# Kernel optimization log

Measured on AMD Instinct MI355X. Metric: run time of the kernel, lower is better.

## Reference

```python
import jax, jax.numpy as jnp
import numpy as np

H, DH = 6, 64
D = H * DH
SQRT_DH = np.float32(np.sqrt(DH))


def _pool_norm(tok, ids):
    # masked mean pooling over tokens, then L2 normalize (Encoder.mean_pooling + normalize)
    mask = (ids > 0).astype(tok.dtype)[:, :, None]
    s = jnp.sum(tok * mask, axis=1) / jnp.clip(jnp.sum(mask, axis=1), 1e-9, None)
    return s / jnp.clip(jnp.linalg.norm(s, axis=1, keepdims=True), 1e-12, None)


def setup_inputs() -> dict:
    key = jax.random.key(0)
    ks = jax.random.split(key, 16)
    N_MSG, N_CON, L, E = 10000, 20000, 16, 128000
    s = 0.05
    eye = jnp.eye(DH, dtype=jnp.float32)
    inp = {}
    inp['tok_msg'] = jax.random.normal(ks[0], (N_MSG, L, D), jnp.float32)
    inp['tok_con'] = jax.random.normal(ks[1], (N_CON, L, D), jnp.float32)
    inp['ids_msg'] = jax.random.randint(ks[2], (N_MSG, L), 0, 100)
    inp['ids_con'] = jax.random.randint(ks[3], (N_CON, L), 0, 100)
    inp['src_cm'] = jax.random.randint(ks[4], (E,), 0, N_CON)
    inp['dst_cm'] = jax.random.randint(ks[5], (E,), 0, N_MSG)
    inp['src_mc'] = jax.random.randint(ks[6], (E,), 0, N_MSG)
    inp['dst_mc'] = jax.random.randint(ks[7], (E,), 0, N_CON)
    inp['lin_W'] = jax.random.normal(ks[8], (2, D, D), jnp.float32) * s
    inp['lin_b'] = jnp.zeros((2, D), jnp.float32)
    inp['kW'] = jax.random.normal(ks[9], (2, 2, D, D), jnp.float32) * s
    inp['kb'] = jnp.zeros((2, 2, D), jnp.float32)
    inp['qW'] = jax.random.normal(ks[10], (2, 2, D, D), jnp.float32) * s
    inp['qb'] = jnp.zeros((2, 2, D), jnp.float32)
    inp['vW'] = jax.random.normal(ks[11], (2, 2, D, D), jnp.float32) * s
    inp['vb'] = jnp.zeros((2, 2, D), jnp.float32)
    inp['aW'] = jax.random.normal(ks[12], (2, 2, D, D), jnp.float32) * s
    inp['ab'] = jnp.zeros((2, 2, D), jnp.float32)
    inp['a_rel'] = jax.random.normal(ks[13], (2, 2, H, DH, DH), jnp.float32) * s + eye
    inp['m_rel'] = jax.random.normal(ks[14], (2, 2, H, DH, DH), jnp.float32) * s + eye
    inp['p_rel'] = jnp.ones((2, 2, H), jnp.float32)
    inp['skip'] = jnp.ones((2, 2), jnp.float32)
    return inp


def _hgt_layer(xs, edges, kW, kb, qW, qb, vW, vb, aW, ab, a_rel, m_rel, p_rel, skip):
    # xs = [x_message, x_concept]; edges = ((src, dst) per edge type)
    k = [(xs[t] @ kW[t] + kb[t]).reshape(-1, H, DH) for t in (0, 1)]
    q = [(xs[t] @ qW[t] + qb[t]).reshape(-1, H, DH) for t in (0, 1)]
    v = [(xs[t] @ vW[t] + vb[t]).reshape(-1, H, DH) for t in (0, 1)]
    edge_meta = ((1, 0), (0, 1))  # edge type e -> (src_type, dst_type)
    agg = [None, None]
    for e, (s, d) in enumerate(edge_meta):
        si, di = edges[e]
        Nd = xs[d].shape[0]
        # relation-specific key/message transforms, per head: [E, H, DH]
        ke = jnp.einsum('ehd,hdf->ehf', k[s][si], a_rel[e])
        score = jnp.einsum('ehf,ehf->eh', q[d][di], ke) * p_rel[e] / SQRT_DH
        # softmax over incoming edges per destination node
        m = jax.ops.segment_max(score, di, num_segments=Nd)
        ex = jnp.exp(score - m[di])
        den = jax.ops.segment_sum(ex, di, num_segments=Nd)
        alpha = ex / den[di]
        msg = jnp.einsum('ehd,hdf->ehf', v[s][si], m_rel[e]) * alpha[:, :, None]
        agg[d] = jax.ops.segment_sum(msg, di, num_segments=Nd).reshape(Nd, D)
    out = []
    for t in (0, 1):
        o = jax.nn.gelu(agg[t], approximate=False) @ aW[t] + ab[t]
        a = jax.nn.sigmoid(skip[t])
        out.append(a * o + (1.0 - a) * xs[t])
    return out


def reference(tok_msg, tok_con, ids_msg, ids_con, src_cm, dst_cm, src_mc, dst_mc,
              lin_W, lin_b, kW, kb, qW, qb, vW, vb, aW, ab, a_rel, m_rel, p_rel, skip):
    x0 = jax.nn.relu(_pool_norm(tok_msg, ids_msg) @ lin_W[0] + lin_b[0])
    x1 = jax.nn.relu(_pool_norm(tok_con, ids_con) @ lin_W[1] + lin_b[1])
    edges = ((src_cm, dst_cm), (src_mc, dst_mc))
    xs = [x0, x1]
    for l in range(2):  # num_layers = 2 (hard-coded in MedicalEncoder)
        xs = _hgt_layer(xs, edges, kW[l], kb[l], qW[l], qb[l], vW[l], vb[l],
                        aW[l], ab[l], a_rel[l], m_rel[l], p_rel[l], skip[l])
    return xs[0]  # x_dict['message']
```

## Files before the change

### kernel.cpp

```cpp
#include <hip/hip_runtime.h>
#include <math.h>

#define H 6
#define DH 64
#define D 384
#define L 16
#define WSZ ((size_t)(D) * (D))
#define RSZ ((size_t)(H) * (DH) * (DH))

typedef __attribute__((ext_vector_type(8))) short short8;
typedef __attribute__((ext_vector_type(4))) float f32x4;
typedef unsigned int uint_;

__device__ __forceinline__ float bf2f(unsigned short u) {
  union { unsigned int i; float f; } x; x.i = ((unsigned int)u) << 16; return x.f;
}
__device__ __forceinline__ unsigned short f2bf(float f) {
  unsigned int x = __float_as_uint(f);
  x = x + 0x7fffu + ((x >> 16) & 1u);
  return (unsigned short)(x >> 16);
}
__device__ __forceinline__ float blo(unsigned int u) { return __uint_as_float(u << 16); }
__device__ __forceinline__ float bhi(unsigned int u) { return __uint_as_float(u & 0xffff0000u); }
__device__ __forceinline__ float geluf(float x) {
  return 0.5f * x * (1.0f + erff(x * 0.70710678118654752f));
}

__global__ void zero_int_kernel(int* p, long n) {
  long i = (long)blockIdx.x * blockDim.x + threadIdx.x;
  long stride = (long)gridDim.x * blockDim.x;
  for (; i < n; i += stride) p[i] = 0;
}

__global__ __launch_bounds__(512) void poolprep_kernel(
    const float* __restrict__ tokM, const int* __restrict__ idsM,
    unsigned short* __restrict__ outM, int NM,
    const float* __restrict__ tokC, const int* __restrict__ idsC,
    unsigned short* __restrict__ outC, int NPOOL,
    const int* __restrict__ dc0, const int* __restrict__ dc1,
    int* __restrict__ deg0, int* __restrict__ deg1, int E, int CH,
    const float* __restrict__ lin_W, const float* __restrict__ kW,
    const float* __restrict__ qW, const float* __restrict__ vW,
    const float* __restrict__ aW, const float* __restrict__ a_rel,
    const float* __restrict__ m_rel, const float* __restrict__ p_rel,
    const float* __restrict__ kb, const float* __restrict__ qb,
    const float* __restrict__ vb,
    unsigned short* __restrict__ wbuf, float* __restrict__ bbuf) {
  __shared__ __align__(16) char smem[16768];
  int t = threadIdx.x;
  if ((int)blockIdx.x < NPOOL) {
    {
      int e = blockIdx.x * CH + t;
      if (t < CH && e < 2 * E) {
        if (e < E) atomicAdd(&deg0[dc0[e]], 1);
        else atomicAdd(&deg1[dc1[e - E]], 1);
      }
    }
    float4 (*part)[96] = (float4(*)[96])smem;
    float* wpart = (float*)(smem + 6144);
    int n = blockIdx.x;
    const float* tok; const int* ids; unsigned short* out;
    if (n < NM) { tok = tokM; ids = idsM; out = outM; }
    else { n -= NM; tok = tokC; ids = idsC; out = outC; }
    int rg = t / 96, c4 = t % 96;
    const float4* tp = (const float4*)(tok + (size_t)n * L * D);
    const int* ip = ids + (size_t)n * L;
    int cnt = 0;
#pragma unroll
    for (int l = 0; l < L; ++l) cnt += (ip[l] > 0);
    float4 s = {0.f, 0.f, 0.f, 0.f};
    if (t < 384) {
#pragma unroll
      for (int li = 0; li < 4; ++li) {
        int l = rg + li * 4;
        if (ip[l] > 0) {
          float4 v = tp[l * 96 + c4];
          s.x += v.x; s.y += v.y; s.z += v.z; s.w += v.w;
        }
      }
      part[rg][c4] = s;
    }
    __syncthreads();
    float4 m4 = {0.f, 0.f, 0.f, 0.f};
    float dot = 0.f;
    float inv_cnt = 1.0f / fmaxf((float)cnt, 1e-9f);
    if (t < 96) {
      float4 a = part[0][t], b = part[1][t], c = part[2][t], d2 = part[3][t];
      m4.x = (a.x + b.x + c.x + d2.x) * inv_cnt;
      m4.y = (a.y + b.y + c.y + d2.y) * inv_cnt;
      m4.z = (a.z + b.z + c.z + d2.z) * inv_cnt;
      m4.w = (a.w + b.w + c.w + d2.w) * inv_cnt;
      dot = m4.x * m4.x + m4.y * m4.y + m4.z * m4.z + m4.w * m4.w;
    }
#pragma unroll
    for (int o = 32; o; o >>= 1) dot += __shfl_down(dot, o);
    if ((t & 63) == 0) wpart[t >> 6] = dot;
    __syncthreads();
    float tot = 0.f;
#pragma unroll
    for (int i = 0; i < 8; ++i) tot += wpart[i];
    float inv = 1.0f / fmaxf(sqrtf(tot), 1e-12f);
    if (t < 96) {
      uint2 o;
      o.x = (uint_)f2bf(m4.x * inv) | ((uint_)f2bf(m4.y * inv) << 16);
      o.y = (uint_)f2bf(m4.z * inv) | ((uint_)f2bf(m4.w * inv) << 16);
      ((uint2*)(out + (size_t)n * D))[t] = o;
    }
    return;
  }
  int q = blockIdx.x - NPOOL;
  if (q >= 14 * 144) {
    int i = (q - 14 * 144) * 512 + t;
    if (i >= 3456) return;
    int gemm, col;
    if (i < 1152) { gemm = 0; col = i; }
    else if (i < 2304) { gemm = 1; col = i - 1152; }
    else if (i < 2688) { gemm = 2; col = i - 2304; }
    else { gemm = 3; col = i - 2688; }
    int sec = col / D, j = col % D, h = j >> 6, rr = j & 63;
    float out = 0.f;
    if (gemm == 0) {
      if (sec == 0) out = kb[j];
      else if (sec == 1) {
        const float* R = a_rel + (size_t)h * 4096 + (size_t)rr * 64;
        float s = 0.f; for (int f = 0; f < 64; ++f) s += qb[h * 64 + f] * R[f];
        out = s * p_rel[h] * 0.125f;
      } else {
        const float* Mm = m_rel + RSZ + (size_t)h * 4096;
        float s = 0.f; for (int d = 0; d < 64; ++d) s += vb[h * 64 + d] * Mm[d * 64 + rr]; out = s;
      }
    } else if (gemm == 1) {
      if (sec == 0) out = kb[D + j];
      else if (sec == 1) {
        const float* R = a_rel + RSZ + (size_t)h * 4096 + (size_t)rr * 64;
        float s = 0.f; for (int f = 0; f < 64; ++f) s += qb[D + h * 64 + f] * R[f];
        out = s * p_rel[H + h] * 0.125f;
      } else {
        const float* Mm = m_rel + (size_t)h * 4096;
        float s = 0.f; for (int d = 0; d < 64; ++d) s += vb[D + h * 64 + d] * Mm[d * 64 + rr]; out = s;
      }
    } else if (gemm == 2) {
      const float* R = a_rel + 2 * RSZ + (size_t)h * 4096 + (size_t)rr * 64;
      float s = 0.f; for (int f = 0; f < 64; ++f) s += qb[2 * D + h * 64 + f] * R[f];
      out = s * p_rel[2 * H + h] * 0.125f;
    } else {
      if (sec == 0) out = kb[3 * D + j];
      else {
        const float* Mm = m_rel + 2 * RSZ + (size_t)h * 4096;
        float s = 0.f; for (int d = 0; d < 64; ++d) s += vb[3 * D + h * 64 + d] * Mm[d * 64 + rr]; out = s;
      }
    }
    bbuf[i] = out;
    return;
  }
  int z = q / 144;
  int r = q % 144;
  int px = r % 12, py = r / 12;
  int tx = t & 31, ty16 = t >> 5;
  const float* src; const float* rel = nullptr; const float* prl = nullptr; int type = 0;
  switch (z) {
    case 0: src = lin_W; break;
    case 1: src = lin_W + WSZ; break;
    case 2: src = kW; break;
    case 3: type = 1; src = qW; rel = a_rel; prl = p_rel; break;
    case 4: type = 2; src = vW; rel = m_rel + RSZ; break;
    case 5: src = kW + WSZ; break;
    case 6: type = 1; src = qW + WSZ; rel = a_rel + RSZ; prl = p_rel + H; break;
    case 7: type = 2; src = vW + WSZ; rel = m_rel; break;
    case 8: type = 1; src = qW + 2 * WSZ; rel = a_rel + 2 * RSZ; prl = p_rel + 2 * H; break;
    case 9: src = kW + 3 * WSZ; break;
    case 10: type = 2; src = vW + 3 * WSZ; rel = m_rel + 2 * RSZ; break;
    case 11: src = aW; break;
    case 12: src = aW + WSZ; break;
    default: src = aW + 2 * WSZ; break;
  }
  unsigned short* dst = wbuf + (size_t)z * WSZ;
  int bx = px * 32;
  int by = py * 32;
  if (type == 0) {
    float (*tile)[33] = (float(*)[33])smem;
#pragma unroll
    for (int s = 0; s < 2; ++s) {
      int r2 = ty16 + s * 16;
      tile[r2][tx] = src[(size_t)(bx + r2) * D + by + tx];
    }
    __syncthreads();
#pragma unroll
    for (int s = 0; s < 2; ++s) {
      int ny = ty16 + s * 16;
      dst[(size_t)(by + ny) * D + bx + tx] = f2bf(tile[tx][ny]);
    }
  } else if (type == 1) {
    float (*Wt_)[65] = (float(*)[65])smem;
    float (*Rt)[65] = (float(*)[65])(smem + 8320);
    int h = by >> 6, d0 = by & 63;
    float sc = prl[h] * 0.125f;
#pragma unroll
    for (int i = 0; i < 4; ++i) {
      int idx = t + i * 512;
      int wr = idx >> 6, wc = idx & 63;
      Wt_[wr][wc] = src[(size_t)(bx + wr) * D + h * 64 + wc];
      Rt[wr][wc] = rel[(size_t)h * 4096 + (size_t)(d0 + wr) * 64 + wc];
    }
    __syncthreads();
#pragma unroll
    for (int s = 0; s < 2; ++s) {
      int ny = ty16 + s * 16;
      float acc = 0.f;
#pragma unroll 16
      for (int f = 0; f < 64; ++f) acc += Wt_[tx][f] * Rt[ny][f];
      dst[(size_t)(by + ny) * D + bx + tx] = f2bf(acc * sc);
    }
  } else {
    float (*Wt2)[65] = (float(*)[65])smem;
    float (*Mt)[33] = (float(*)[33])(smem + 8320);
    int h = by >> 6, f0 = by & 63;
#pragma unroll
    for (int i = 0; i < 4; ++i) {
      int idx = t + i * 512;
      int wr = idx >> 6, wc = idx & 63;
      Wt2[wr][wc] = src[(size_t)(bx + wr) * D + h * 64 + wc];
      int dr = idx >> 5, fc = idx & 31;
      Mt[dr][fc] = rel[(size_t)h * 4096 + (size_t)dr * 64 + f0 + fc];
    }
    __syncthreads();
#pragma unroll
    for (int s = 0; s < 2; ++s) {
      int ny = ty16 + s * 16;
      float acc = 0.f;
#pragma unroll 16
      for (int d = 0; d < 64; ++d) acc += Wt2[tx][d] * Mt[d][ny];
      dst[(size_t)(by + ny) * D + bx + tx] = f2bf(acc);
    }
  }
}

__global__ void scan2_kernel(const int* __restrict__ deg0, int* __restrict__ off0, int N0,
                             const int* __restrict__ deg1, int* __restrict__ off1, int N1) {
  const int* deg = blockIdx.x ? deg1 : deg0;
  int* off = blockIdx.x ? off1 : off0;
  int N = blockIdx.x ? N1 : N0;
  __shared__ int wsum[16];
  __shared__ int carrySh;
  int tid = threadIdx.x;
  int lane = tid & 63, wid = tid >> 6;
  if (tid == 0) carrySh = 0;
  __syncthreads();
  for (int base = 0; base < N; base += 1024) {
    int i = base + tid;
    int v = (i < N) ? deg[i] : 0;
    int s = v;
#pragma unroll
    for (int o = 1; o < 64; o <<= 1) {
      int t2 = __shfl_up(s, o);
      if (lane >= o) s += t2;
    }
    if (lane == 63) wsum[wid] = s;
    __syncthreads();
    int wpre = 0;
    for (int j = 0; j < wid; ++j) wpre += wsum[j];
    int c = carrySh;
    if (i < N) off[i] = c + wpre + s - v;
    __syncthreads();
    if (tid == 1023) carrySh = c + wpre + s;
    __syncthreads();
  }
  if (tid == 0) off[N] = carrySh;
}

struct AttnP {
  const unsigned short* kb;
  const unsigned short* tqb;
  const unsigned short* vmb;
  const int* off;
  const int* elist;
  unsigned short* aggb;
  int N, sk, st, sv, nb;
};

__global__ void attn_kernel(AttnP a0, AttnP a1) {
  bool first = (int)blockIdx.x < a0.nb;
  AttnP a = first ? a0 : a1;
  int bx = first ? (int)blockIdx.x : (int)blockIdx.x - a0.nb;
  int node = bx * 4 + (threadIdx.x >> 6);
  int lane = threadIdx.x & 63;
  if (node >= a.N) return;
  int e0 = a.off[node], e1 = a.off[node + 1];
  const uint_* tq32 = (const uint_*)(a.tqb + (size_t)node * a.st);
  float tq0[3], tq1[3], m[3], den[3], ac0[3], ac1[3];
#pragma unroll
  for (int j = 0; j < 3; ++j) {
    uint_ u = tq32[lane + 64 * j];
    tq0[j] = blo(u); tq1[j] = bhi(u);
    m[j] = -1e30f; den[j] = 0.f; ac0[j] = 0.f; ac1[j] = 0.f;
  }
  int i = e0;
  for (; i + 2 <= e1; i += 2) {
    int s0 = a.elist[i], s1 = a.elist[i + 1];
    const uint_* k0 = (const uint_*)(a.kb + (size_t)s0 * a.sk);
    const uint_* k1 = (const uint_*)(a.kb + (size_t)s1 * a.sk);
    const uint_* v0 = (const uint_*)(a.vmb + (size_t)s0 * a.sv);
    const uint_* v1 = (const uint_*)(a.vmb + (size_t)s1 * a.sv);
    float pa[3], pb[3]; uint_ va[3], vb[3];
#pragma unroll
    for (int j = 0; j < 3; ++j) {
      uint_ ka = k0[lane + 64 * j], kbu = k1[lane + 64 * j];
      va[j] = v0[lane + 64 * j]; vb[j] = v1[lane + 64 * j];
      pa[j] = blo(ka) * tq0[j] + bhi(ka) * tq1[j];
      pb[j] = blo(kbu) * tq0[j] + bhi(kbu) * tq1[j];
    }
#pragma unroll
    for (int o = 1; o <= 16; o <<= 1)
#pragma unroll
      for (int j = 0; j < 3; ++j) {
        pa[j] += __shfl_xor(pa[j], o);
        pb[j] += __shfl_xor(pb[j], o);
      }
#pragma unroll
    for (int j = 0; j < 3; ++j) {
      float mn = fmaxf(m[j], fmaxf(pa[j], pb[j]));
      float r = __expf(m[j] - mn);
      float p0 = __expf(pa[j] - mn);
      float p1 = __expf(pb[j] - mn);
      den[j] = den[j] * r + p0 + p1;
      ac0[j] = ac0[j] * r + p0 * blo(va[j]) + p1 * blo(vb[j]);
      ac1[j] = ac1[j] * r + p0 * bhi(va[j]) + p1 * bhi(vb[j]);
      m[j] = mn;
    }
  }
  if (i < e1) {
    int s0 = a.elist[i];
    const uint_* k0 = (const uint_*)(a.kb + (size_t)s0 * a.sk);
    const uint_* v0 = (const uint_*)(a.vmb + (size_t)s0 * a.sv);
    float pa[3]; uint_ va[3];
#pragma unroll
    for (int j = 0; j < 3; ++j) {
      uint_ ka = k0[lane + 64 * j];
      va[j] = v0[lane + 64 * j];
      pa[j] = blo(ka) * tq0[j] + bhi(ka) * tq1[j];
    }
#pragma unroll
    for (int o = 1; o <= 16; o <<= 1)
#pragma unroll
      for (int j = 0; j < 3; ++j) pa[j] += __shfl_xor(pa[j], o);
#pragma unroll
    for (int j = 0; j < 3; ++j) {
      float mn = fmaxf(m[j], pa[j]);
      float r = __expf(m[j] - mn);
      float p0 = __expf(pa[j] - mn);
      den[j] = den[j] * r + p0;
      ac0[j] = ac0[j] * r + p0 * blo(va[j]);
      ac1[j] = ac1[j] * r + p0 * bhi(va[j]);
      m[j] = mn;
    }
  }
  uint_* op32 = (uint_*)(a.aggb + (size_t)node * D);
#pragma unroll
  for (int j = 0; j < 3; ++j) {
    float o0 = (e1 > e0) ? ac0[j] / den[j] : 0.f;
    float o1 = (e1 > e0) ? ac1[j] / den[j] : 0.f;
    op32[lane + 64 * j] = (uint_)f2bf(geluf(o0)) | ((uint_)f2bf(geluf(o1)) << 16);
  }
}

struct GemmP {
  const unsigned short* A;
  const unsigned short* Wt;
  const float* bias;
  float* Cf;
  unsigned short* Cb;
  const unsigned short* xold;
  const float* skipPtr;
  int M, N, cpitch, relu;
};
struct ScatP {
  const int *d0, *s0, *off0;
  int *cur0, *el0;
  const int *d1, *s1, *off1;
  int *cur1, *el1;
  int E;
};

__global__ __launch_bounds__(256) void gemm_bf16(GemmP q0, GemmP q1, ScatP sc) {
  if (blockIdx.z == 2) {
    int nb = gridDim.x * gridDim.y;
    int flat = blockIdx.y * gridDim.x + blockIdx.x;
    for (int e = flat * 256 + threadIdx.x; e < 2 * sc.E; e += nb * 256) {
      if (e < sc.E) {
        int d = sc.d0[e];
        sc.el0[sc.off0[d] + atomicAdd(&sc.cur0[d], 1)] = sc.s0[e];
      } else {
        int ee = e - sc.E;
        int d = sc.d1[ee];
        sc.el1[sc.off1[d] + atomicAdd(&sc.cur1[d], 1)] = sc.s1[ee];
      }
    }
    return;
  }
  GemmP p = blockIdx.z ? q1 : q0;
  const int bm = blockIdx.x * 128, bn = blockIdx.y * 128;
  if (bm >= p.M || bn >= p.N) return;
  __shared__ __align__(16) unsigned short As[2][128 * 64];
  __shared__ __align__(16) unsigned short Bs[2][128 * 64];
  const int tid = threadIdx.x;
  const int w = tid >> 6, lane = tid & 63;

  auto stage = [&](int t, int buf) {
#pragma unroll
    for (int i = 0; i < 4; ++i) {
      int cid = (w * 4 + i) * 64 + lane;
      int row = cid >> 3;
      int cg = (cid & 7) ^ (row & 7);
      int grow = bm + row;
      if (grow >= p.M) grow = p.M - 1;
      const unsigned short* gp = p.A + (size_t)grow * D + t * 64 + cg * 8;
      __builtin_amdgcn_global_load_lds((const __attribute__((address_space(1))) void*)gp,
                                       (__attribute__((address_space(3))) void*)&As[buf][(w * 4 + i) * 512],
                                       16, 0, 0);
    }
#pragma unroll
    for (int i = 0; i < 4; ++i) {
      int cid = (w * 4 + i) * 64 + lane;
      int row = cid >> 3;
      int cg = (cid & 7) ^ (row & 7);
      const unsigned short* gp = p.Wt + (size_t)(bn + row) * D + t * 64 + cg * 8;
      __builtin_amdgcn_global_load_lds((const __attribute__((address_space(1))) void*)gp,
                                       (__attribute__((address_space(3))) void*)&Bs[buf][(w * 4 + i) * 512],
                                       16, 0, 0);
    }
  };

  stage(0, 0);
  __syncthreads();

  const int wr = w >> 1, wc = w & 1;
  const int la = lane & 15, hi = lane >> 4;
  f32x4 acc[4][4] = {};

  for (int t = 0; t < 6; ++t) {
    if (t < 5) stage(t + 1, (t + 1) & 1);
    const unsigned short* Ab = As[t & 1];
    const unsigned short* Bb = Bs[t & 1];
#pragma unroll
    for (int ks = 0; ks < 2; ++ks) {
      int c = ks * 4 + hi;
      short8 af[4], bfr[4];
#pragma unroll
      for (int mi = 0; mi < 4; ++mi) {
        int row = wr * 64 + mi * 16 + la;
        af[mi] = *(const short8*)&Ab[row * 64 + ((c ^ (row & 7)) * 8)];
      }
#pragma unroll
      for (int n = 0; n < 4; ++n) {
        int col = wc * 64 + n * 16 + la;
        bfr[n] = *(const short8*)&Bb[col * 64 + ((c ^ (col & 7)) * 8)];
      }
#pragma unroll
      for (int mi = 0; mi < 4; ++mi)
#pragma unroll
        for (int n = 0; n < 4; ++n)
          acc[mi][n] = __builtin_amdgcn_mfma_f32_16x16x32_bf16(af[mi], bfr[n], acc[mi][n], 0, 0, 0);
    }
    __syncthreads();
  }

  float sa = 0.f;
  if (p.xold) sa = 1.0f / (1.0f + __expf(-*p.skipPtr));
#pragma unroll
  for (int mi = 0; mi < 4; ++mi) {
#pragma unroll
    for (int n = 0; n < 4; ++n) {
#pragma unroll
      for (int r = 0; r < 4; ++r) {
        int row = bm + wr * 64 + mi * 16 + hi * 4 + r;
        int col = bn + wc * 64 + n * 16 + la;
        if (row >= p.M) continue;
        float v = acc[mi][n][r] + p.bias[col];
        if (p.relu) v = fmaxf(v, 0.f);
        if (p.xold) v = sa * v + (1.0f - sa) * bf2f(p.xold[(size_t)row * D + col]);
        if (p.Cf) p.Cf[(size_t)row * p.cpitch + col] = v;
        if (p.Cb) p.Cb[(size_t)row * p.cpitch + col] = f2bf(v);
      }
    }
  }
}

extern "C" void kernel_launch(void* const* d_in, const int* in_sizes, int n_in,
                              void* d_out, int out_size, void* d_ws, size_t ws_size,
                              hipStream_t stream) {
  const float* tok_msg = (const float*)d_in[0];
  const float* tok_con = (const float*)d_in[1];
  const int* ids_msg = (const int*)d_in[2];
  const int* ids_con = (const int*)d_in[3];
  const int* src_cm = (const int*)d_in[4];
  const int* dst_cm = (const int*)d_in[5];
  const int* src_mc = (const int*)d_in[6];
  const int* dst_mc = (const int*)d_in[7];
  const float* lin_W = (const float*)d_in[8];
  const float* lin_b = (const float*)d_in[9];
  const float* kW = (const float*)d_in[10];
  const float* kb = (const float*)d_in[11];
  const float* qW = (const float*)d_in[12];
  const float* qb = (const float*)d_in[13];
  const float* vW = (const float*)d_in[14];
  const float* vb = (const float*)d_in[15];
  const float* aW = (const float*)d_in[16];
  const float* ab = (const float*)d_in[17];
  const float* a_rel = (const float*)d_in[18];
  const float* m_rel = (const float*)d_in[19];
  const float* p_rel = (const float*)d_in[20];
  const float* skip = (const float*)d_in[21];

  const int NM = in_sizes[2] / L;
  const int NC = in_sizes[3] / L;
  const int E = in_sizes[4];

  char* wsb = (char*)d_ws;
  size_t woff = 0;
  auto alloc = [&](size_t bytes) {
    woff = (woff + 255) & ~(size_t)255;
    void* p = wsb + woff;
    woff += bytes;
    return p;
  };
  const size_t NMe = (size_t)NM * D, NCe = (size_t)NC * D;
  unsigned short* poolM = (unsigned short*)alloc(NMe * 2);
  unsigned short* poolC = (unsigned short*)alloc(NCe * 2);
  unsigned short* x0b = (unsigned short*)alloc(NMe * 2);
  unsigned short* x1b = (unsigned short*)alloc(NCe * 2);
  unsigned short* xn0b = (unsigned short*)alloc(NMe * 2);
  unsigned short* xn1b = (unsigned short*)alloc(NCe * 2);
  unsigned short* projM1 = (unsigned short*)alloc((size_t)NM * 1152 * 2);
  unsigned short* projC1 = (unsigned short*)alloc((size_t)NC * 1152 * 2);
  unsigned short* projM2 = (unsigned short*)alloc((size_t)NM * 384 * 2);
  unsigned short* projC2 = (unsigned short*)alloc((size_t)NC * 768 * 2);
  unsigned short* aggM = (unsigned short*)alloc(NMe * 2);
  unsigned short* aggC = (unsigned short*)alloc(NCe * 2);
  unsigned short* wbuf = (unsigned short*)alloc(14 * WSZ * 2);
  float* bbuf = (float*)alloc(3456 * 4);
  long nz = 2L * NM + 2L * NC;
  int* ibase = (int*)alloc((size_t)(nz + NM + 1 + NC + 1 + 2L * E) * 4);
  int* deg0 = ibase;
  int* cur0 = deg0 + NM;
  int* deg1 = cur0 + NM;
  int* cur1 = deg1 + NC;
  int* off0 = cur1 + NC;
  int* off1 = off0 + NM + 1;
  int* el0 = off1 + NC + 1;
  int* el1 = el0 + E;

  dim3 b256(256);
  const int mbM = (NM + 127) / 128, mbC = (NC + 127) / 128;
  const int mbMax = (mbM > mbC) ? mbM : mbC;
  ScatP scNone = {};
  ScatP scAll = {dst_cm, src_cm, off0, cur0, el0, dst_mc, src_mc, off1, cur1, el1, E};

  zero_int_kernel<<<64, b256, 0, stream>>>(ibase, nz);

  const int NPOOL = NM + NC;
  const int CH = (2 * E + NPOOL - 1) / NPOOL;
  poolprep_kernel<<<NPOOL + 14 * 144 + 7, 512, 0, stream>>>(
      tok_msg, ids_msg, poolM, NM, tok_con, ids_con, poolC, NPOOL,
      dst_cm, dst_mc, deg0, deg1, E, CH,
      lin_W, kW, qW, vW, aW, a_rel, m_rel, p_rel, kb, qb, vb, wbuf, bbuf);

  scan2_kernel<<<2, 1024, 0, stream>>>(deg0, off0, NM, deg1, off1, NC);

  {
    GemmP p0 = {poolM, wbuf, lin_b, nullptr, x0b, nullptr, nullptr, NM, D, D, 1};
    GemmP p1 = {poolC, wbuf + WSZ, lin_b + D, nullptr, x1b, nullptr, nullptr, NC, D, D, 1};
    gemm_bf16<<<dim3(mbMax, 3, 3), b256, 0, stream>>>(p0, p1, scAll);
  }
  {
    GemmP p0 = {x0b, wbuf + 2 * WSZ, bbuf, nullptr, projM1, nullptr, nullptr, NM, 1152, 1152, 0};
    GemmP p1 = {x1b, wbuf + 5 * WSZ, bbuf + 1152, nullptr, projC1, nullptr, nullptr, NC, 1152, 1152, 0};
    gemm_bf16<<<dim3(mbMax, 9, 2), b256, 0, stream>>>(p0, p1, scNone);
  }
  {
    AttnP a0 = {projC1, projM1 + 384, projC1 + 768, off0, el0, aggM, NM, 1152, 1152, 1152, (NM + 3) / 4};
    AttnP a1 = {projM1, projC1 + 384, projM1 + 768, off1, el1, aggC, NC, 1152, 1152, 1152, (NC + 3) / 4};
    attn_kernel<<<(NM + 3) / 4 + (NC + 3) / 4, b256, 0, stream>>>(a0, a1);
  }
  {
    GemmP p0 = {aggM, wbuf + 11 * WSZ, ab, nullptr, xn0b, x0b, skip + 0, NM, D, D, 0};
    GemmP p1 = {aggC, wbuf + 12 * WSZ, ab + D, nullptr, xn1b, x1b, skip + 1, NC, D, D, 0};
    gemm_bf16<<<dim3(mbMax, 3, 2), b256, 0, stream>>>(p0, p1, scNone);
  }
  {
    GemmP p0 = {xn0b, wbuf + 8 * WSZ, bbuf + 2304, nullptr, projM2, nullptr, nullptr, NM, 384, 384, 0};
    GemmP p1 = {xn1b, wbuf + 9 * WSZ, bbuf + 2688, nullptr, projC2, nullptr, nullptr, NC, 768, 768, 0};
    gemm_bf16<<<dim3(mbMax, 6, 2), b256, 0, stream>>>(p0, p1, scNone);
  }
  {
    AttnP a0 = {projC2, projM2, projC2 + 384, off0, el0, aggM, NM, 768, 384, 768, (NM + 3) / 4};
    AttnP a1 = a0;
    attn_kernel<<<(NM + 3) / 4, b256, 0, stream>>>(a0, a1);
  }
  {
    GemmP p0 = {aggM, wbuf + 13 * WSZ, ab + 2 * D, (float*)d_out, nullptr, xn0b, skip + 2, NM, D, D, 0};
    GemmP p1 = p0;
    gemm_bf16<<<dim3(mbM, 3, 1), b256, 0, stream>>>(p0, p1, scNone);
  }
}
```

Before: 628.2 us.

## Fuse GEMM and attention stages into one cooperative persistent kernel

Replaces the six separate GEMM and attention launches with a single cooperative mega-kernel. It loops over tiles or nodes persistently and separates stages with grid-wide syncs. This removes per-launch overhead and tail gaps between stages. In exchange, the grid is capped at 512 blocks, which may reduce occupancy and latency hiding in the gather-heavy attention and GEMM phases. The old multi-launch path is kept as a fallback if the cooperative launch fails.

```diff
diff --git a/kernel.cpp b/kernel.cpp
--- a/kernel.cpp
+++ b/kernel.cpp
@@ -1,5 +1,8 @@
 #include <hip/hip_runtime.h>
+#include <hip/hip_cooperative_groups.h>
 #include <math.h>
+
+namespace coop = cooperative_groups;
 
 #define H 6
 #define DH 64
@@ -268,102 +271,7 @@
   if (tid == 0) off[N] = carrySh;
 }
 
-struct AttnP {
-  const unsigned short* kb;
-  const unsigned short* tqb;
-  const unsigned short* vmb;
-  const int* off;
-  const int* elist;
-  unsigned short* aggb;
-  int N, sk, st, sv, nb;
-};
-
-__global__ void attn_kernel(AttnP a0, AttnP a1) {
-  bool first = (int)blockIdx.x < a0.nb;
-  AttnP a = first ? a0 : a1;
-  int bx = first ? (int)blockIdx.x : (int)blockIdx.x - a0.nb;
-  int node = bx * 4 + (threadIdx.x >> 6);
-  int lane = threadIdx.x & 63;
-  if (node >= a.N) return;
-  int e0 = a.off[node], e1 = a.off[node + 1];
-  const uint_* tq32 = (const uint_*)(a.tqb + (size_t)node * a.st);
-  float tq0[3], tq1[3], m[3], den[3], ac0[3], ac1[3];
-#pragma unroll
-  for (int j = 0; j < 3; ++j) {
-    uint_ u = tq32[lane + 64 * j];
-    tq0[j] = blo(u); tq1[j] = bhi(u);
-    m[j] = -1e30f; den[j] = 0.f; ac0[j] = 0.f; ac1[j] = 0.f;
-  }
-  int i = e0;
-  for (; i + 2 <= e1; i += 2) {
-    int s0 = a.elist[i], s1 = a.elist[i + 1];
-    const uint_* k0 = (const uint_*)(a.kb + (size_t)s0 * a.sk);
-    const uint_* k1 = (const uint_*)(a.kb + (size_t)s1 * a.sk);
-    const uint_* v0 = (const uint_*)(a.vmb + (size_t)s0 * a.sv);
-    const uint_* v1 = (const uint_*)(a.vmb + (size_t)s1 * a.sv);
-    float pa[3], pb[3]; uint_ va[3], vb[3];
-#pragma unroll
-    for (int j = 0; j < 3; ++j) {
-      uint_ ka = k0[lane + 64 * j], kbu = k1[lane + 64 * j];
-      va[j] = v0[lane + 64 * j]; vb[j] = v1[lane + 64 * j];
-      pa[j] = blo(ka) * tq0[j] + bhi(ka) * tq1[j];
-      pb[j] = blo(kbu) * tq0[j] + bhi(kbu) * tq1[j];
-    }
-#pragma unroll
-    for (int o = 1; o <= 16; o <<= 1)
-#pragma unroll
-      for (int j = 0; j < 3; ++j) {
-        pa[j] += __shfl_xor(pa[j], o);
-        pb[j] += __shfl_xor(pb[j], o);
-      }
-#pragma unroll
-    for (int j = 0; j < 3; ++j) {
-      float mn = fmaxf(m[j], fmaxf(pa[j], pb[j]));
-      float r = __expf(m[j] - mn);
-      float p0 = __expf(pa[j] - mn);
-      float p1 = __expf(pb[j] - mn);
-      den[j] = den[j] * r + p0 + p1;
-      ac0[j] = ac0[j] * r + p0 * blo(va[j]) + p1 * blo(vb[j]);
-      ac1[j] = ac1[j] * r + p0 * bhi(va[j]) + p1 * bhi(vb[j]);
-      m[j] = mn;
-    }
-  }
-  if (i < e1) {
-    int s0 = a.elist[i];
-    const uint_* k0 = (const uint_*)(a.kb + (size_t)s0 * a.sk);
-    const uint_* v0 = (const uint_*)(a.vmb + (size_t)s0 * a.sv);
-    float pa[3]; uint_ va[3];
-#pragma unroll
-    for (int j = 0; j < 3; ++j) {
-      uint_ ka = k0[lane + 64 * j];
-      va[j] = v0[lane + 64 * j];
-      pa[j] = blo(ka) * tq0[j] + bhi(ka) * tq1[j];
-    }
-#pragma unroll
-    for (int o = 1; o <= 16; o <<= 1)
-#pragma unroll
-      for (int j = 0; j < 3; ++j) pa[j] += __shfl_xor(pa[j], o);
-#pragma unroll
-    for (int j = 0; j < 3; ++j) {
-      float mn = fmaxf(m[j], pa[j]);
-      float r = __expf(m[j] - mn);
-      float p0 = __expf(pa[j] - mn);
-      den[j] = den[j] * r + p0;
-      ac0[j] = ac0[j] * r + p0 * blo(va[j]);
-      ac1[j] = ac1[j] * r + p0 * bhi(va[j]);
-      m[j] = mn;
-    }
-  }
-  uint_* op32 = (uint_*)(a.aggb + (size_t)node * D);
-#pragma unroll
-  for (int j = 0; j < 3; ++j) {
-    float o0 = (e1 > e0) ? ac0[j] / den[j] : 0.f;
-    float o1 = (e1 > e0) ? ac1[j] / den[j] : 0.f;
-    op32[lane + 64 * j] = (uint_)f2bf(geluf(o0)) | ((uint_)f2bf(geluf(o1)) << 16);
-  }
-}
-
-struct GemmP {
+struct GP {
   const unsigned short* A;
   const unsigned short* Wt;
   const float* bias;
@@ -381,25 +289,7 @@
   int E;
 };
 
-__global__ __launch_bounds__(256) void gemm_bf16(GemmP q0, GemmP q1, ScatP sc) {
-  if (blockIdx.z == 2) {
-    int nb = gridDim.x * gridDim.y;
-    int flat = blockIdx.y * gridDim.x + blockIdx.x;
-    for (int e = flat * 256 + threadIdx.x; e < 2 * sc.E; e += nb * 256) {
-      if (e < sc.E) {
-        int d = sc.d0[e];
-        sc.el0[sc.off0[d] + atomicAdd(&sc.cur0[d], 1)] = sc.s0[e];
-      } else {
-        int ee = e - sc.E;
-        int d = sc.d1[ee];
-        sc.el1[sc.off1[d] + atomicAdd(&sc.cur1[d], 1)] = sc.s1[ee];
-      }
-    }
-    return;
-  }
-  GemmP p = blockIdx.z ? q1 : q0;
-  const int bm = blockIdx.x * 128, bn = blockIdx.y * 128;
-  if (bm >= p.M || bn >= p.N) return;
+__device__ void gemm_tile(const GP& p, int bm, int bn) {
   __shared__ __align__(16) unsigned short As[2][128 * 64];
   __shared__ __align__(16) unsigned short Bs[2][128 * 64];
   const int tid = threadIdx.x;
@@ -410,10 +300,10 @@
     for (int i = 0; i < 4; ++i) {
       int cid = (w * 4 + i) * 64 + lane;
       int row = cid >> 3;
-      int cg = (cid & 7) ^ (row & 7);
+      int cg2 = (cid & 7) ^ (row & 7);
       int grow = bm + row;
       if (grow >= p.M) grow = p.M - 1;
-      const unsigned short* gp = p.A + (size_t)grow * D + t * 64 + cg * 8;
+      const unsigned short* gp = p.A + (size_t)grow * D + t * 64 + cg2 * 8;
       __builtin_amdgcn_global_load_lds((const __attribute__((address_space(1))) void*)gp,
                                        (__attribute__((address_space(3))) void*)&As[buf][(w * 4 + i) * 512],
                                        16, 0, 0);
@@ -422,8 +312,8 @@
     for (int i = 0; i < 4; ++i) {
       int cid = (w * 4 + i) * 64 + lane;
       int row = cid >> 3;
-      int cg = (cid & 7) ^ (row & 7);
-      const unsigned short* gp = p.Wt + (size_t)(bn + row) * D + t * 64 + cg * 8;
+      int cg2 = (cid & 7) ^ (row & 7);
+      const unsigned short* gp = p.Wt + (size_t)(bn + row) * D + t * 64 + cg2 * 8;
       __builtin_amdgcn_global_load_lds((const __attribute__((address_space(1))) void*)gp,
                                        (__attribute__((address_space(3))) void*)&Bs[buf][(w * 4 + i) * 512],
                                        16, 0, 0);
@@ -448,7 +338,7 @@
 #pragma unroll
       for (int mi = 0; mi < 4; ++mi) {
         int row = wr * 64 + mi * 16 + la;
-        af[mi] = *(const short8*)&Ab[row * 64 + ((c ^ (row & 7)) * 8)];
+        af[mi] = *(const short8*)&As[t & 1][row * 64 + ((c ^ (row & 7)) * 8)];
       }
 #pragma unroll
       for (int n = 0; n < 4; ++n) {
@@ -482,6 +372,233 @@
         if (p.Cb) p.Cb[(size_t)row * p.cpitch + col] = f2bf(v);
       }
     }
+  }
+}
+
+struct AttnP {
+  const unsigned short* kb;
+  const unsigned short* tqb;
+  const unsigned short* vmb;
+  const int* off;
+  const int* elist;
+  unsigned short* aggb;
+  int N, sk, st, sv, nb;
+};
+
+__device__ void attn_node(const AttnP& a, int node) {
+  int lane = threadIdx.x & 63;
+  int e0 = a.off[node], e1 = a.off[node + 1];
+  const uint_* tq32 = (const uint_*)(a.tqb + (size_t)node * a.st);
+  float tq0[3], tq1[3], m[3], den[3], ac0[3], ac1[3];
+#pragma unroll
+  for (int j = 0; j < 3; ++j) {
+    uint_ u = tq32[lane + 64 * j];
+    tq0[j] = blo(u); tq1[j] = bhi(u);
+    m[j] = -1e30f; den[j] = 0.f; ac0[j] = 0.f; ac1[j] = 0.f;
+  }
+  int i = e0;
+  for (; i + 2 <= e1; i += 2) {
+    int s0 = a.elist[i], s1 = a.elist[i + 1];
+    const uint_* k0 = (const uint_*)(a.kb + (size_t)s0 * a.sk);
+    const uint_* k1 = (const uint_*)(a.kb + (size_t)s1 * a.sk);
+    const uint_* v0 = (const uint_*)(a.vmb + (size_t)s0 * a.sv);
+    const uint_* v1 = (const uint_*)(a.vmb + (size_t)s1 * a.sv);
+    float pa[3], pb[3]; uint_ va[3], vb[3];
+#pragma unroll
+    for (int j = 0; j < 3; ++j) {
+      uint_ ka = k0[lane + 64 * j], kbu = k1[lane + 64 * j];
+      va[j] = v0[lane + 64 * j]; vb[j] = v1[lane + 64 * j];
+      pa[j] = blo(ka) * tq0[j] + bhi(ka) * tq1[j];
+      pb[j] = blo(kbu) * tq0[j] + bhi(kbu) * tq1[j];
+    }
+#pragma unroll
+    for (int o = 1; o <= 16; o <<= 1)
+#pragma unroll
+      for (int j = 0; j < 3; ++j) {
+        pa[j] += __shfl_xor(pa[j], o);
+        pb[j] += __shfl_xor(pb[j], o);
+      }
+#pragma unroll
+    for (int j = 0; j < 3; ++j) {
+      float mn = fmaxf(m[j], fmaxf(pa[j], pb[j]));
+      float r = __expf(m[j] - mn);
+      float p0 = __expf(pa[j] - mn);
+      float p1 = __expf(pb[j] - mn);
+      den[j] = den[j] * r + p0 + p1;
+      ac0[j] = ac0[j] * r + p0 * blo(va[j]) + p1 * blo(vb[j]);
+      ac1[j] = ac1[j] * r + p0 * bhi(va[j]) + p1 * bhi(vb[j]);
+      m[j] = mn;
+    }
+  }
+  if (i < e1) {
+    int s0 = a.elist[i];
+    const uint_* k0 = (const uint_*)(a.kb + (size_t)s0 * a.sk);
+    const uint_* v0 = (const uint_*)(a.vmb + (size_t)s0 * a.sv);
+    float pa[3]; uint_ va[3];
+#pragma unroll
+    for (int j = 0; j < 3; ++j) {
+      uint_ ka = k0[lane + 64 * j];
+      va[j] = v0[lane + 64 * j];
+      pa[j] = blo(ka) * tq0[j] + bhi(ka) * tq1[j];
+    }
+#pragma unroll
+    for (int o = 1; o <= 16; o <<= 1)
+#pragma unroll
+      for (int j = 0; j < 3; ++j) pa[j] += __shfl_xor(pa[j], o);
+#pragma unroll
+    for (int j = 0; j < 3; ++j) {
+      float mn = fmaxf(m[j], pa[j]);
+      float r = __expf(m[j] - mn);
+      float p0 = __expf(pa[j] - mn);
+      den[j] = den[j] * r + p0;
+      ac0[j] = ac0[j] * r + p0 * blo(va[j]);
+      ac1[j] = ac1[j] * r + p0 * bhi(va[j]);
+      m[j] = mn;
+    }
+  }
+  uint_* op32 = (uint_*)(a.aggb + (size_t)node * D);
+#pragma unroll
+  for (int j = 0; j < 3; ++j) {
+    float o0 = (e1 > e0) ? ac0[j] / den[j] : 0.f;
+    float o1 = (e1 > e0) ? ac1[j] / den[j] : 0.f;
+    op32[lane + 64 * j] = (uint_)f2bf(geluf(o0)) | ((uint_)f2bf(geluf(o1)) << 16);
+  }
+}
+
+__global__ __launch_bounds__(256) void gemm_std(GP q0, GP q1, ScatP sc) {
+  if (blockIdx.z == 2) {
+    int nb = gridDim.x * gridDim.y;
+    int flat = blockIdx.y * gridDim.x + blockIdx.x;
+    for (long e = (long)flat * 256 + threadIdx.x; e < 2L * sc.E; e += (long)nb * 256) {
+      if (e < sc.E) {
+        int d = sc.d0[e];
+        sc.el0[sc.off0[d] + atomicAdd(&sc.cur0[d], 1)] = sc.s0[e];
+      } else {
+        long ee = e - sc.E;
+        int d = sc.d1[ee];
+        sc.el1[sc.off1[d] + atomicAdd(&sc.cur1[d], 1)] = sc.s1[ee];
+      }
+    }
+    return;
+  }
+  GP p = blockIdx.z ? q1 : q0;
+  const int bm = blockIdx.x * 128, bn = blockIdx.y * 128;
+  if (bm >= p.M || bn >= p.N) return;
+  gemm_tile(p, bm, bn);
+}
+
+__global__ void attn_std(AttnP a0, AttnP a1) {
+  bool first = (int)blockIdx.x < a0.nb;
+  AttnP a = first ? a0 : a1;
+  int bx = first ? (int)blockIdx.x : (int)blockIdx.x - a0.nb;
+  int node = bx * 4 + (threadIdx.x >> 6);
+  if (node < a.N) attn_node(a, node);
+}
+
+struct MegaArgs {
+  const unsigned short *poolM, *poolC;
+  unsigned short *x0b, *x1b, *xn0b, *xn1b;
+  unsigned short *projM1, *projC1, *projM2, *projC2;
+  unsigned short *aggM, *aggC;
+  const unsigned short* wbuf;
+  const float *bbuf, *lin_b, *ab, *skip;
+  float* out;
+  const int *off0, *off1;
+  int *el0, *el1, *cur0, *cur1;
+  const int *dst_cm, *src_cm, *dst_mc, *src_mc;
+  int NM, NC, E;
+};
+
+__device__ __forceinline__ void gemm_stage2(const GP& p0, const GP& p1, int mb0, int mb1) {
+  int nt0 = mb0 * (p0.N / 128), nt1 = mb1 * (p1.N / 128);
+  for (int t = blockIdx.x; t < nt0 + nt1; t += gridDim.x) {
+    if (t < nt0) gemm_tile(p0, (t % mb0) * 128, (t / mb0) * 128);
+    else { int u = t - nt0; gemm_tile(p1, (u % mb1) * 128, (u / mb1) * 128); }
+  }
+}
+
+__device__ __forceinline__ void attn_stage2(const AttnP& a0, const AttnP& a1) {
+  int wv = threadIdx.x >> 6;
+  for (int g = blockIdx.x; g < a0.nb + a1.nb; g += gridDim.x) {
+    const AttnP& a = (g < a0.nb) ? a0 : a1;
+    int gg = (g < a0.nb) ? g : g - a0.nb;
+    int node = gg * 4 + wv;
+    if (node < a.N) attn_node(a, node);
+  }
+}
+
+__global__ __launch_bounds__(256) void mega_kernel(MegaArgs A) {
+  coop::grid_group grid = coop::this_grid();
+  const int mbM = (A.NM + 127) / 128, mbC = (A.NC + 127) / 128;
+
+  {
+    GP p0 = {A.poolM, A.wbuf, A.lin_b, nullptr, A.x0b, nullptr, nullptr, A.NM, D, D, 1};
+    GP p1 = {A.poolC, A.wbuf + WSZ, A.lin_b + D, nullptr, A.x1b, nullptr, nullptr, A.NC, D, D, 1};
+    int nt0 = mbM * 3, nt1 = mbC * 3;
+    const int ST = 256;
+    for (int t = blockIdx.x; t < nt0 + nt1 + ST; t += gridDim.x) {
+      if (t < nt0) gemm_tile(p0, (t % mbM) * 128, (t / mbM) * 128);
+      else if (t < nt0 + nt1) { int u = t - nt0; gemm_tile(p1, (u % mbC) * 128, (u / mbC) * 128); }
+      else {
+        int u = t - nt0 - nt1;
+        for (long e = (long)u * 256 + threadIdx.x; e < 2L * A.E; e += (long)ST * 256) {
+          if (e < A.E) {
+            int d = A.dst_cm[e];
+            A.el0[A.off0[d] + atomicAdd(&A.cur0[d], 1)] = A.src_cm[e];
+          } else {
+            long ee = e - A.E;
+            int d = A.dst_mc[ee];
+            A.el1[A.off1[d] + atomicAdd(&A.cur1[d], 1)] = A.src_mc[ee];
+          }
+        }
+      }
+    }
+  }
+  __threadfence();
+  grid.sync();
+  {
+    GP p0 = {A.x0b, A.wbuf + 2 * WSZ, A.bbuf, nullptr, A.projM1, nullptr, nullptr, A.NM, 1152, 1152, 0};
+    GP p1 = {A.x1b, A.wbuf + 5 * WSZ, A.bbuf + 1152, nullptr, A.projC1, nullptr, nullptr, A.NC, 1152, 1152, 0};
+    gemm_stage2(p0, p1, mbM, mbC);
+  }
+  __threadfence();
+  grid.sync();
+  {
+    AttnP a0 = {A.projC1, A.projM1 + 384, A.projC1 + 768, A.off0, A.el0, A.aggM, A.NM, 1152, 1152, 1152, (A.NM + 3) / 4};
+    AttnP a1 = {A.projM1, A.projC1 + 384, A.projM1 + 768, A.off1, A.el1, A.aggC, A.NC, 1152, 1152, 1152, (A.NC + 3) / 4};
+    attn_stage2(a0, a1);
+  }
+  __threadfence();
+  grid.sync();
+  {
+    GP p0 = {A.aggM, A.wbuf + 11 * WSZ, A.ab, nullptr, A.xn0b, A.x0b, A.skip + 0, A.NM, D, D, 0};
+    GP p1 = {A.aggC, A.wbuf + 12 * WSZ, A.ab + D, nullptr, A.xn1b, A.x1b, A.skip + 1, A.NC, D, D, 0};
+    gemm_stage2(p0, p1, mbM, mbC);
+  }
+  __threadfence();
+  grid.sync();
+  {
+    GP p0 = {A.xn0b, A.wbuf + 8 * WSZ, A.bbuf + 2304, nullptr, A.projM2, nullptr, nullptr, A.NM, 384, 384, 0};
+    GP p1 = {A.xn1b, A.wbuf + 9 * WSZ, A.bbuf + 2688, nullptr, A.projC2, nullptr, nullptr, A.NC, 768, 768, 0};
+    gemm_stage2(p0, p1, mbM, mbC);
+  }
+  __threadfence();
+  grid.sync();
+  {
+    AttnP a0 = {A.projC2, A.projM2, A.projC2 + 384, A.off0, A.el0, A.aggM, A.NM, 768, 384, 768, (A.NM + 3) / 4};
+    int wv = threadIdx.x >> 6;
+    for (int g = blockIdx.x; g < a0.nb; g += gridDim.x) {
+      int node = g * 4 + wv;
+      if (node < a0.N) attn_node(a0, node);
+    }
+  }
+  __threadfence();
+  grid.sync();
+  {
+    GP p0 = {A.aggM, A.wbuf + 13 * WSZ, A.ab + 2 * D, A.out, nullptr, A.xn0b, A.skip + 2, A.NM, D, D, 0};
+    int nt0 = mbM * 3;
+    for (int t = blockIdx.x; t < nt0; t += gridDim.x)
+      gemm_tile(p0, (t % mbM) * 128, (t / mbM) * 128);
   }
 }
 
@@ -552,8 +669,6 @@
   dim3 b256(256);
   const int mbM = (NM + 127) / 128, mbC = (NC + 127) / 128;
   const int mbMax = (mbM > mbC) ? mbM : mbC;
-  ScatP scNone = {};
-  ScatP scAll = {dst_cm, src_cm, off0, cur0, el0, dst_mc, src_mc, off1, cur1, el1, E};
 
   zero_int_kernel<<<64, b256, 0, stream>>>(ibase, nz);
 
@@ -566,39 +681,64 @@
 
   scan2_kernel<<<2, 1024, 0, stream>>>(deg0, off0, NM, deg1, off1, NC);
 
-  {
-    GemmP p0 = {poolM, wbuf, lin_b, nullptr, x0b, nullptr, nullptr, NM, D, D, 1};
-    GemmP p1 = {poolC, wbuf + WSZ, lin_b + D, nullptr, x1b, nullptr, nullptr, NC, D, D, 1};
-    gemm_bf16<<<dim3(mbMax, 3, 3), b256, 0, stream>>>(p0, p1, scAll);
-  }
-  {
-    GemmP p0 = {x0b, wbuf + 2 * WSZ, bbuf, nullptr, projM1, nullptr, nullptr, NM, 1152, 1152, 0};
-    GemmP p1 = {x1b, wbuf + 5 * WSZ, bbuf + 1152, nullptr, projC1, nullptr, nullptr, NC, 1152, 1152, 0};
-    gemm_bf16<<<dim3(mbMax, 9, 2), b256, 0, stream>>>(p0, p1, scNone);
-  }
-  {
-    AttnP a0 = {projC1, projM1 + 384, projC1 + 768, off0, el0, aggM, NM, 1152, 1152, 1152, (NM + 3) / 4};
-    AttnP a1 = {projM1, projC1 + 384, projM1 + 768, off1, el1, aggC, NC, 1152, 1152, 1152, (NC + 3) / 4};
-    attn_kernel<<<(NM + 3) / 4 + (NC + 3) / 4, b256, 0, stream>>>(a0, a1);
-  }
-  {
-    GemmP p0 = {aggM, wbuf + 11 * WSZ, ab, nullptr, xn0b, x0b, skip + 0, NM, D, D, 0};
-    GemmP p1 = {aggC, wbuf + 12 * WSZ, ab + D, nullptr, xn1b, x1b, skip + 1, NC, D, D, 0};
-    gemm_bf16<<<dim3(mbMax, 3, 2), b256, 0, stream>>>(p0, p1, scNone);
-  }
-  {
-    GemmP p0 = {xn0b, wbuf + 8 * WSZ, bbuf + 2304, nullptr, projM2, nullptr, nullptr, NM, 384, 384, 0};
-    GemmP p1 = {xn1b, wbuf + 9 * WSZ, bbuf + 2688, nullptr, projC2, nullptr, nullptr, NC, 768, 768, 0};
-    gemm_bf16<<<dim3(mbMax, 6, 2), b256, 0, stream>>>(p0, p1, scNone);
-  }
-  {
-    AttnP a0 = {projC2, projM2, projC2 + 384, off0, el0, aggM, NM, 768, 384, 768, (NM + 3) / 4};
-    AttnP a1 = a0;
-    attn_kernel<<<(NM + 3) / 4, b256, 0, stream>>>(a0, a1);
-  }
-  {
-    GemmP p0 = {aggM, wbuf + 13 * WSZ, ab + 2 * D, (float*)d_out, nullptr, xn0b, skip + 2, NM, D, D, 0};
-    GemmP p1 = p0;
-    gemm_bf16<<<dim3(mbM, 3, 1), b256, 0, stream>>>(p0, p1, scNone);
-  }
-}
+  MegaArgs ma;
+  ma.poolM = poolM; ma.poolC = poolC;
+  ma.x0b = x0b; ma.x1b = x1b; ma.xn0b = xn0b; ma.xn1b = xn1b;
+  ma.projM1 = projM1; ma.projC1 = projC1; ma.projM2 = projM2; ma.projC2 = projC2;
+  ma.aggM = aggM; ma.aggC = aggC;
+  ma.wbuf = wbuf; ma.bbuf = bbuf; ma.lin_b = lin_b; ma.ab = ab; ma.skip = skip;
+  ma.out = (float*)d_out;
+  ma.off0 = off0; ma.off1 = off1; ma.el0 = el0; ma.el1 = el1;
+  ma.cur0 = cur0; ma.cur1 = cur1;
+  ma.dst_cm = dst_cm; ma.src_cm = src_cm; ma.dst_mc = dst_mc; ma.src_mc = src_mc;
+  ma.NM = NM; ma.NC = NC; ma.E = E;
+  void* kargs[] = {(void*)&ma};
+
+  hipError_t ce = hipLaunchCooperativeKernel((const void*)mega_kernel, dim3(512), dim3(256),
+                                             kargs, 0, stream);
+  if (ce != hipSuccess) {
+    (void)hipGetLastError();
+    ce = hipLaunchCooperativeKernel((const void*)mega_kernel, dim3(256), dim3(256),
+                                    kargs, 0, stream);
+  }
+  if (ce != hipSuccess) {
+    (void)hipGetLastError();
+    ScatP scNone = {};
+    ScatP scAll = {dst_cm, src_cm, off0, cur0, el0, dst_mc, src_mc, off1, cur1, el1, E};
+    {
+      GP p0 = {poolM, wbuf, lin_b, nullptr, x0b, nullptr, nullptr, NM, D, D, 1};
+      GP p1 = {poolC, wbuf + WSZ, lin_b + D, nullptr, x1b, nullptr, nullptr, NC, D, D, 1};
+      gemm_std<<<dim3(mbMax, 3, 3), b256, 0, stream>>>(p0, p1, scAll);
+    }
+    {
+      GP p0 = {x0b, wbuf + 2 * WSZ, bbuf, nullptr, projM1, nullptr, nullptr, NM, 1152, 1152, 0};
+      GP p1 = {x1b, wbuf + 5 * WSZ, bbuf + 1152, nullptr, projC1, nullptr, nullptr, NC, 1152, 1152, 0};
+      gemm_std<<<dim3(mbMax, 9, 2), b256, 0, stream>>>(p0, p1, scNone);
+    }
+    {
+      AttnP a0 = {projC1, projM1 + 384, projC1 + 768, off0, el0, aggM, NM, 1152, 1152, 1152, (NM + 3) / 4};
+      AttnP a1 = {projM1, projC1 + 384, projM1 + 768, off1, el1, aggC, NC, 1152, 1152, 1152, (NC + 3) / 4};
+      attn_std<<<(NM + 3) / 4 + (NC + 3) / 4, b256, 0, stream>>>(a0, a1);
+    }
+    {
+      GP p0 = {aggM, wbuf + 11 * WSZ, ab, nullptr, xn0b, x0b, skip + 0, NM, D, D, 0};
+      GP p1 = {aggC, wbuf + 12 * WSZ, ab + D, nullptr, xn1b, x1b, skip + 1, NC, D, D, 0};
+      gemm_std<<<dim3(mbMax, 3, 2), b256, 0, stream>>>(p0, p1, scNone);
+    }
+    {
+      GP p0 = {xn0b, wbuf + 8 * WSZ, bbuf + 2304, nullptr, projM2, nullptr, nullptr, NM, 384, 384, 0};
+      GP p1 = {xn1b, wbuf + 9 * WSZ, bbuf + 2688, nullptr, projC2, nullptr, nullptr, NC, 768, 768, 0};
+      gemm_std<<<dim3(mbMax, 6, 2), b256, 0, stream>>>(p0, p1, scNone);
+    }
+    {
+      AttnP a0 = {projC2, projM2, projC2 + 384, off0, el0, aggM, NM, 768, 384, 768, (NM + 3) / 4};
+      AttnP a1 = a0;
+      attn_std<<<(NM + 3) / 4, b256, 0, stream>>>(a0, a1);
+    }
+    {
+      GP p0 = {aggM, wbuf + 13 * WSZ, ab + 2 * D, (float*)d_out, nullptr, xn0b, skip + 2, NM, D, D, 0};
+      GP p1 = p0;
+      gemm_std<<<dim3(mbM, 3, 1), b256, 0, stream>>>(p0, p1, scNone);
+    }
+  }
+}
```

New measurement: 1.594 ms. 154% more time.
